# Optimization experiments

Hardware: AMD Instinct MI355X
Metric: run time of the kernel (lower is better)

## Reference

```python
import jax, jax.numpy as jnp
import numpy as np

N_NODES = 10000
N_EDGES = 160000
F_IN, D1, D2, D_OUT, K = 512, 512, 512, 256, 3


def _gcn_layer(x, row, col, w, W, b, n):
    # PyG GCNConv (improved=False): add self-loops with weight 1, sym norm.
    loop = jnp.arange(n)
    r = jnp.concatenate([row, loop])
    c = jnp.concatenate([col, loop])
    ww = jnp.concatenate([w, jnp.ones((n,), w.dtype)])
    deg = jax.ops.segment_sum(ww, c, num_segments=n)
    dinv = jnp.where(deg > 0, jax.lax.rsqrt(deg), 0.0)
    norm = dinv[r] * ww * dinv[c]              # [E+N]
    h = x @ W                                  # dense GEMM first (as PyG lin)
    out = jax.ops.segment_sum(norm[:, None] * h[r], c, num_segments=n)
    return out + b


def _cheb_layer(x, row, col, w, Wk, b, n):
    # PyG ChebConv, normalization='sym', lambda_max=2.0:
    # L_hat = 2L/lmax - I = -D^{-1/2} A D^{-1/2} (self-loops removed first).
    w0 = jnp.where(row == col, jnp.zeros((), w.dtype), w)  # remove self loops
    deg = jax.ops.segment_sum(w0, row, num_segments=n)
    dinv = jnp.where(deg > 0, jax.lax.rsqrt(deg), 0.0)
    norm = dinv[row] * w0 * dinv[col]          # [E]

    def lhat(z):  # L_hat @ z
        return -jax.ops.segment_sum(norm[:, None] * z[row], col, num_segments=n)

    Tx0 = x
    out = Tx0 @ Wk[0]
    Tx1 = lhat(x)
    out = out + Tx1 @ Wk[1]
    for k in range(2, Wk.shape[0]):            # static K, fine to unroll
        Tx2 = 2.0 * lhat(Tx1) - Tx0
        out = out + Tx2 @ Wk[k]
        Tx0, Tx1 = Tx1, Tx2
    return out + b


def setup_inputs() -> dict:
    key = jax.random.key(0)
    ks = jax.random.split(key, 9)
    x = jax.random.normal(ks[0], (N_NODES, F_IN), dtype=jnp.float32)
    edge_index = jax.random.randint(ks[1], (2, N_EDGES), 0, N_NODES, dtype=jnp.int64)
    edge_weight = jax.random.uniform(ks[2], (N_EDGES,), dtype=jnp.float32)
    s = lambda fan: 1.0 / np.sqrt(fan)
    W1 = jax.random.normal(ks[3], (F_IN, D1), dtype=jnp.float32) * s(F_IN)
    b1 = jnp.zeros((D1,), jnp.float32)
    W2 = jax.random.normal(ks[4], (D1, D2), dtype=jnp.float32) * s(D1)
    b2 = jnp.zeros((D2,), jnp.float32)
    Wc = jax.random.normal(ks[5], (K, D2, D_OUT), dtype=jnp.float32) * s(D2)
    bc = jnp.zeros((D_OUT,), jnp.float32)
    return {"x": x, "edge_index": edge_index, "edge_weight": edge_weight,
            "W1": W1, "b1": b1, "W2": W2, "b2": b2, "Wc": Wc, "bc": bc}


def reference(x, edge_index, edge_weight, W1, b1, W2, b2, Wc, bc):
    row, col = edge_index[0], edge_index[1]
    n = x.shape[0]
    h = jax.nn.celu(_gcn_layer(x, row, col, edge_weight, W1, b1, n))
    h = jax.nn.celu(_gcn_layer(h, row, col, edge_weight, W2, b2, n))
    h = jax.nn.celu(_cheb_layer(h, row, col, edge_weight, Wc, bc, n))
    return h
```

## Files before the change

kernel.cpp:

```cpp
#include <hip/hip_runtime.h>
#include <math.h>

#define N_NODES 10000
#define N_EDGES 160000
#define FDIM    512
#define DOUT    256
#define NCAT    768

typedef unsigned short ushort_t;
typedef unsigned int   uint_t;
typedef __attribute__((ext_vector_type(8))) short bf16x8;
typedef __attribute__((ext_vector_type(4))) float f32x4;

__device__ inline ushort_t f2bf(float f) {
    uint_t u = __float_as_uint(f);
    u += 0x7fffu + ((u >> 16) & 1u);
    return (ushort_t)(u >> 16);
}
__device__ inline void bf2f8(uint4 u, float* v) {
    v[0] = __uint_as_float(u.x << 16); v[1] = __uint_as_float(u.x & 0xffff0000u);
    v[2] = __uint_as_float(u.y << 16); v[3] = __uint_as_float(u.y & 0xffff0000u);
    v[4] = __uint_as_float(u.z << 16); v[5] = __uint_as_float(u.z & 0xffff0000u);
    v[6] = __uint_as_float(u.w << 16); v[7] = __uint_as_float(u.w & 0xffff0000u);
}
__device__ inline uint4 f2bf8v(const float* v) {
    uint4 u;
    u.x = (uint_t)f2bf(v[0]) | ((uint_t)f2bf(v[1]) << 16);
    u.y = (uint_t)f2bf(v[2]) | ((uint_t)f2bf(v[3]) << 16);
    u.z = (uint_t)f2bf(v[4]) | ((uint_t)f2bf(v[5]) << 16);
    u.w = (uint_t)f2bf(v[6]) | ((uint_t)f2bf(v[7]) << 16);
    return u;
}
__device__ inline void gld_lds16(const ushort_t* g, ushort_t* l) {
    __builtin_amdgcn_global_load_lds(
        (const __attribute__((address_space(1))) unsigned int*)g,
        (__attribute__((address_space(3))) unsigned int*)l,
        16, 0, 0);
}

#define EDGE_BLOCKS 625
#define XB_BLOCKS   5000

__global__ __launch_bounds__(256) void k_pre1(
    const int* __restrict__ row, const int* __restrict__ col,
    const float* __restrict__ w,
    float* deg_g, float* deg_c, int* counts,
    const float* __restrict__ x,  ushort_t* __restrict__ xb,
    const float* __restrict__ W1, ushort_t* __restrict__ W1t,
    const float* __restrict__ W2, ushort_t* __restrict__ W2t,
    const float* __restrict__ Wc, ushort_t* __restrict__ Wcatt)
{
    __shared__ float tile[64][65];
    int b = blockIdx.x;
    int tid = threadIdx.x;
    if (b < EDGE_BLOCKS) {
        int e = b * 256 + tid;
        if (e < N_EDGES) {
            int r = row[e], c = col[e];
            float wv = w[e];
            atomicAdd(&deg_g[c], wv);
            if (r != c) atomicAdd(&deg_c[r], wv);
            atomicAdd(&counts[c], 1);
        }
        return;
    }
    b -= EDGE_BLOCKS;
    if (b < XB_BLOCKS) {
        int t = b * 256 + tid;
        float4 v = *(const float4*)(x + (size_t)t * 4);
        uint2 p;
        p.x = (uint_t)f2bf(v.x) | ((uint_t)f2bf(v.y) << 16);
        p.y = (uint_t)f2bf(v.z) | ((uint_t)f2bf(v.w) << 16);
        *(uint2*)(xb + (size_t)t * 4) = p;
        return;
    }
    b -= XB_BLOCKS;
    const float* src; const float* src2 = nullptr;
    ushort_t* dst; int kt, ntG, srcld;
    if (b < 64) {
        kt = b >> 3; ntG = b & 7; srcld = FDIM;
        src = W1 + (size_t)(kt * 64) * FDIM + ntG * 64;
        dst = W1t;
    } else if (b < 128) {
        int bb = b - 64;
        kt = bb >> 3; ntG = bb & 7; srcld = FDIM;
        src = W2 + (size_t)(kt * 64) * FDIM + ntG * 64;
        dst = W2t;
    } else {
        int bb = b - 128;
        ntG = bb / 8; kt = bb % 8; srcld = DOUT;
        int s = ntG >> 2;
        int nl = (ntG & 3) * 64;
        if (s == 0) {
            src  = Wc + (size_t)(kt * 64) * DOUT + nl;
            src2 = Wc + (size_t)2 * FDIM * DOUT + (size_t)(kt * 64) * DOUT + nl;
        } else if (s == 1) {
            src  = Wc + (size_t)1 * FDIM * DOUT + (size_t)(kt * 64) * DOUT + nl;
        } else {
            src  = Wc + (size_t)2 * FDIM * DOUT + (size_t)(kt * 64) * DOUT + nl;
        }
        dst = Wcatt;
    }
    {
        int r = tid >> 2, c0 = (tid & 3) * 16;
        const float* sp = src + (size_t)r * srcld + c0;
#pragma unroll
        for (int q = 0; q < 4; ++q) {
            float4 a = *(const float4*)(sp + q * 4);
            if (src2) {
                float4 bsub = *(const float4*)(src2 + (size_t)r * srcld + c0 + q * 4);
                a.x -= bsub.x; a.y -= bsub.y; a.z -= bsub.z; a.w -= bsub.w;
            }
            tile[r][c0 + q * 4 + 0] = a.x;
            tile[r][c0 + q * 4 + 1] = a.y;
            tile[r][c0 + q * 4 + 2] = a.z;
            tile[r][c0 + q * 4 + 3] = a.w;
        }
    }
    __syncthreads();
    {
        int n = tid >> 2, k0 = (tid & 3) * 16;
        float v[16];
#pragma unroll
        for (int i = 0; i < 16; ++i) v[i] = tile[k0 + i][n];
        uint4 u0 = f2bf8v(v);
        uint4 u1 = f2bf8v(v + 8);
        ushort_t* dp = dst + (size_t)(ntG * 64 + n) * FDIM + kt * 64 + k0;
        *(uint4*)dp = u0;
        *(uint4*)(dp + 8) = u1;
    }
}

__global__ __launch_bounds__(256) void k_dinv_scan1(
    const float* __restrict__ deg_g, const float* __restrict__ deg_c,
    float* __restrict__ dinv_g, float* __restrict__ dinv_c,
    const int* __restrict__ counts, int* __restrict__ rp,
    int* __restrict__ part, int n)
{
    __shared__ int s[256];
    int tid = threadIdx.x;
    int i = blockIdx.x * 256 + tid;
    if (i < n) {
        dinv_g[i] = rsqrtf(deg_g[i] + 1.0f);
        float d = deg_c[i];
        dinv_c[i] = d > 0.f ? rsqrtf(d) : 0.f;
    }
    int v = (i < n) ? counts[i] : 0;
    s[tid] = v;
    __syncthreads();
    for (int o = 1; o < 256; o <<= 1) {
        int t = (tid >= o) ? s[tid - o] : 0;
        __syncthreads();
        s[tid] += t;
        __syncthreads();
    }
    if (i < n) rp[i] = s[tid] - v;
    if (tid == 255) part[blockIdx.x] = s[255];
}

__global__ __launch_bounds__(256) void k_scan23(int* __restrict__ rp,
                                                const int* __restrict__ part,
                                                int nb, int n) {
    __shared__ int soff[64];
    __shared__ int stot;
    int tid = threadIdx.x;
    if (tid < 64) {
        int v = (tid < nb) ? part[tid] : 0;
        int x = v;
        for (int o = 1; o < 64; o <<= 1) {
            int y = __shfl_up(x, o, 64);
            if (tid >= o) x += y;
        }
        soff[tid] = x - v;
        if (tid == 63) stot = x;
    }
    __syncthreads();
    int i = blockIdx.x * 256 + tid;
    if (i < n) rp[i] += soff[blockIdx.x];
    if (blockIdx.x == 0 && tid == 0) rp[n] = stot;
}

__global__ void k_fill(const int* __restrict__ row, const int* __restrict__ col,
                       const float* __restrict__ w,
                       const float* __restrict__ dinv_g, const float* __restrict__ dinv_c,
                       const int* __restrict__ rp, int* __restrict__ fill,
                       int2* __restrict__ eg, int2* __restrict__ ec, int E) {
    int e = blockIdx.x * blockDim.x + threadIdx.x;
    if (e >= E) return;
    int r = row[e], c = col[e];
    float wv = w[e];
    float ng = dinv_g[r] * wv * dinv_g[c];
    float w0 = (r == c) ? 0.f : wv;
    float nc = -(dinv_c[r] * w0 * dinv_c[c]);
    int pos = rp[c] + atomicAdd(&fill[c], 1);
    eg[pos] = make_int2(r, __float_as_int(ng));
    ec[pos] = make_int2(r, __float_as_int(nc));
}

__global__ __launch_bounds__(256) void k_mgemm(
    const ushort_t* __restrict__ A, int lda,
    const ushort_t* __restrict__ Bt, int ldb,
    int M, int K, int N, int nbx, int nby,
    ushort_t* __restrict__ outB)
{
    __shared__ ushort_t As[64 * 32];
    __shared__ ushort_t Bs[128 * 32];

    int id = blockIdx.x;
    int j = id & 7, t = id >> 3;
    int by = t % nby;
    int bx = (t / nby) * 8 + j;
    if (bx >= nbx) return;

    const int tid  = threadIdx.x;
    const int w    = tid >> 6;
    const int lane = tid & 63;
    const int l15  = lane & 15;
    const int quad = lane >> 4;
    const int bm = bx * 64, bn = by * 128;
    const int wm = (w & 1) * 32;
    const int wn = (w >> 1) * 64;

    const int sr = lane >> 2;
    const int sc = (lane & 3) * 8;
    int arow = min(bm + w * 16 + sr, M - 1);
    const ushort_t* ag = A + (size_t)arow * lda + sc;
    ushort_t* al = As + (w * 16 + sr) * 32 + sc;
    const ushort_t* bg0 = Bt + (size_t)(bn + w * 32 + sr) * ldb + sc;
    const ushort_t* bg1 = bg0 + (size_t)16 * ldb;
    ushort_t* bl0 = Bs + (w * 32 + sr) * 32 + sc;
    ushort_t* bl1 = bl0 + 16 * 32;

    f32x4 acc[2][4] = {};

    for (int k0 = 0; k0 < K; k0 += 32) {
        __syncthreads();
        gld_lds16(ag + k0, al);
        gld_lds16(bg0 + k0, bl0);
        gld_lds16(bg1 + k0, bl1);
        __syncthreads();
        bf16x8 af[2], bfr[4];
#pragma unroll
        for (int i = 0; i < 2; ++i)
            af[i] = *(const bf16x8*)(As + (wm + i * 16 + l15) * 32 + quad * 8);
#pragma unroll
        for (int jj = 0; jj < 4; ++jj)
            bfr[jj] = *(const bf16x8*)(Bs + (wn + jj * 16 + l15) * 32 + quad * 8);
#pragma unroll
        for (int i = 0; i < 2; ++i)
#pragma unroll
            for (int jj = 0; jj < 4; ++jj)
                acc[i][jj] = __builtin_amdgcn_mfma_f32_16x16x32_bf16(af[i], bfr[jj], acc[i][jj], 0, 0, 0);
    }

#pragma unroll
    for (int i = 0; i < 2; ++i) {
        int rowb = bm + wm + i * 16 + quad * 4;
#pragma unroll
        for (int jj = 0; jj < 4; ++jj) {
            int col = bn + wn + jj * 16 + l15;
#pragma unroll
            for (int r = 0; r < 4; ++r) {
                int rr = rowb + r;
                if (rr < M)
                    outB[(size_t)rr * N + col] = f2bf(acc[i][jj][r]);
            }
        }
    }
}

template<int SL>
__global__ __launch_bounds__(256) void k_sagg(
    const ushort_t* __restrict__ h, int hs, int hoff,
    const int2* __restrict__ er, const int* __restrict__ rp,
    const float* __restrict__ dinv_g,
    const ushort_t* __restrict__ other, int os, int ooff, float sB,
    const float* __restrict__ bias, float sA,
    ushort_t* __restrict__ outB, float* __restrict__ outF, int outs, int celu)
{
    const int id  = blockIdx.x;
    const int sl  = id % SL;
    const int tid = threadIdx.x;
    const int c   = (id / SL) * 32 + (tid >> 3);
    if (c >= N_NODES) return;
    const int f = sl * 64 + ((tid & 7) << 3);
    const ushort_t* hp = h + hoff + f;

    float acc[8] = {0.f, 0.f, 0.f, 0.f, 0.f, 0.f, 0.f, 0.f};
    int e = rp[c];
    const int e1 = rp[c + 1];
    for (; e + 4 <= e1; e += 4) {
        int2 p0 = er[e], p1 = er[e + 1], p2 = er[e + 2], p3 = er[e + 3];
        uint4 u0 = *(const uint4*)(hp + (size_t)p0.x * hs);
        uint4 u1 = *(const uint4*)(hp + (size_t)p1.x * hs);
        uint4 u2 = *(const uint4*)(hp + (size_t)p2.x * hs);
        uint4 u3 = *(const uint4*)(hp + (size_t)p3.x * hs);
        float n0 = __int_as_float(p0.y), n1 = __int_as_float(p1.y);
        float n2 = __int_as_float(p2.y), n3 = __int_as_float(p3.y);
        float v0[8], v1[8], v2[8], v3[8];
        bf2f8(u0, v0); bf2f8(u1, v1); bf2f8(u2, v2); bf2f8(u3, v3);
#pragma unroll
        for (int i = 0; i < 8; ++i) {
            acc[i] = fmaf(n0, v0[i], acc[i]);
            acc[i] = fmaf(n1, v1[i], acc[i]);
            acc[i] = fmaf(n2, v2[i], acc[i]);
            acc[i] = fmaf(n3, v3[i], acc[i]);
        }
    }
    for (; e < e1; ++e) {
        int2 p = er[e];
        uint4 u = *(const uint4*)(hp + (size_t)p.x * hs);
        float nv = __int_as_float(p.y);
        float v[8]; bf2f8(u, v);
#pragma unroll
        for (int i = 0; i < 8; ++i) acc[i] = fmaf(nv, v[i], acc[i]);
    }

    if (dinv_g) {
        float dv = dinv_g[c];
        float d2 = dv * dv;
        uint4 u = *(const uint4*)(hp + (size_t)c * hs);
        float v[8]; bf2f8(u, v);
#pragma unroll
        for (int i = 0; i < 8; ++i) acc[i] = fmaf(d2, v[i], acc[i]);
    }
    float r[8];
#pragma unroll
    for (int i = 0; i < 8; ++i) r[i] = sA * acc[i];
    if (other) {
        uint4 u = *(const uint4*)(other + (size_t)c * os + ooff + f);
        float o[8]; bf2f8(u, o);
#pragma unroll
        for (int i = 0; i < 8; ++i) r[i] = fmaf(sB, o[i], r[i]);
    }
    if (bias) {
#pragma unroll
        for (int i = 0; i < 8; ++i) r[i] += bias[f + i];
    }
    if (celu) {
#pragma unroll
        for (int i = 0; i < 8; ++i) r[i] = r[i] > 0.f ? r[i] : expm1f(r[i]);
    }
    if (outF) {
        float* op = outF + (size_t)c * outs + f;
        *(float4*)op       = make_float4(r[0], r[1], r[2], r[3]);
        *(float4*)(op + 4) = make_float4(r[4], r[5], r[6], r[7]);
    } else {
        *(uint4*)(outB + (size_t)c * outs + f) = f2bf8v(r);
    }
}


extern "C" void kernel_launch(void* const* d_in, const int* in_sizes, int n_in,
                              void* d_out, int out_size, void* d_ws, size_t ws_size,
                              hipStream_t stream) {
    const float* x  = (const float*)d_in[0];
    const int*   ei = (const int*)d_in[1];
    const float* ew = (const float*)d_in[2];
    const float* W1 = (const float*)d_in[3];
    const float* b1 = (const float*)d_in[4];
    const float* W2 = (const float*)d_in[5];
    const float* b2 = (const float*)d_in[6];
    const float* Wc = (const float*)d_in[7];
    const float* bc = (const float*)d_in[8];
    float* out = (float*)d_out;

    const int* row = ei;
    const int* col = ei + N_EDGES;

    char* ws = (char*)d_ws;
    size_t off = 0;
    auto alloc = [&](size_t bytes) -> void* {
        void* p = ws + off;
        off += (bytes + 255) & ~(size_t)255;
        return p;
    };
    ushort_t* xb    = (ushort_t*)alloc((size_t)N_NODES * FDIM * 2);
    ushort_t* bufA  = (ushort_t*)alloc((size_t)N_NODES * FDIM * 2);
    ushort_t* bufB  = (ushort_t*)alloc((size_t)N_NODES * FDIM * 2);
    ushort_t* Y     = (ushort_t*)alloc((size_t)N_NODES * NCAT * 2);
    ushort_t* P     = (ushort_t*)alloc((size_t)N_NODES * DOUT * 2);
    ushort_t* W1t   = (ushort_t*)alloc((size_t)FDIM * FDIM * 2);
    ushort_t* W2t   = (ushort_t*)alloc((size_t)FDIM * FDIM * 2);
    ushort_t* Wcatt = (ushort_t*)alloc((size_t)NCAT * FDIM * 2);
    size_t zs = off;
    float* deg_g  = (float*)alloc((size_t)N_NODES * 4);
    float* deg_c  = (float*)alloc((size_t)N_NODES * 4);
    int*   counts = (int*)alloc((size_t)N_NODES * 4);
    int*   fillb  = (int*)alloc((size_t)N_NODES * 4);
    size_t ze = off;
    float* dinv_g = (float*)alloc((size_t)N_NODES * 4);
    float* dinv_c = (float*)alloc((size_t)N_NODES * 4);
    int*   rp     = (int*)alloc((size_t)(N_NODES + 1) * 4);
    int*   part   = (int*)alloc(64 * 4);
    int2*  eg     = (int2*)alloc((size_t)N_EDGES * 8);
    int2*  ec     = (int2*)alloc((size_t)N_EDGES * 8);

    const int TB = 256;
    dim3 edgeGrid((N_EDGES + TB - 1) / TB);
    int nScanB = (N_NODES + 255) / 256;

    hipMemsetAsync(ws + zs, 0, ze - zs, stream);
    k_pre1<<<EDGE_BLOCKS + XB_BLOCKS + 224, 256, 0, stream>>>(
        row, col, ew, deg_g, deg_c, counts,
        x, xb, W1, W1t, W2, W2t, Wc, Wcatt);
    k_dinv_scan1<<<nScanB, 256, 0, stream>>>(deg_g, deg_c, dinv_g, dinv_c, counts, rp, part, N_NODES);
    k_scan23<<<nScanB, 256, 0, stream>>>(rp, part, nScanB, N_NODES);
    k_fill<<<edgeGrid, TB, 0, stream>>>(row, col, ew, dinv_g, dinv_c, rp, fillb, eg, ec, N_EDGES);

    auto mgemm = [&](const ushort_t* A, const ushort_t* Bt, int N, ushort_t* oB) {
        int nbx = (N_NODES + 63) / 64, nby = N / 128;
        int G = 8 * (((nbx + 7) / 8) * nby);
        k_mgemm<<<G, 256, 0, stream>>>(A, FDIM, Bt, FDIM, N_NODES, FDIM, N, nbx, nby, oB);
    };
    int g8 = ((N_NODES + 31) / 32) * 8;
    int g4 = ((N_NODES + 31) / 32) * 4;

    mgemm(xb, W1t, FDIM, bufA);
    k_sagg<8><<<g8, 256, 0, stream>>>(bufA, FDIM, 0, eg, rp, dinv_g,
                                      (const ushort_t*)nullptr, 0, 0, 0.f,
                                      b1, 1.f, bufB, (float*)nullptr, FDIM, 1);
    mgemm(bufB, W2t, FDIM, bufA);
    k_sagg<8><<<g8, 256, 0, stream>>>(bufA, FDIM, 0, eg, rp, dinv_g,
                                      (const ushort_t*)nullptr, 0, 0, 0.f,
                                      b2, 1.f, bufB, (float*)nullptr, FDIM, 1);
    mgemm(bufB, Wcatt, NCAT, Y);
    k_sagg<4><<<g4, 256, 0, stream>>>(Y, NCAT, 2 * DOUT, ec, rp,
                                      (const float*)nullptr,
                                      Y, NCAT, DOUT, 1.f,
                                      (const float*)nullptr, 2.f,
                                      P, (float*)nullptr, DOUT, 0);
    k_sagg<4><<<g4, 256, 0, stream>>>(P, DOUT, 0, ec, rp,
                                      (const float*)nullptr,
                                      Y, NCAT, 0, 1.f,
                                      bc, 1.f,
                                      (ushort_t*)nullptr, out, DOUT, 1);
}
```

Before: 239.7 us.

## Fuse all stages into one cooperative persistent megakernel with grid syncs

Replaces the sequence of preprocessing, GEMM and aggregation kernel launches with a single cooperative persistent kernel. Its blocks loop over virtual block ids and separate the phases with grid-wide barriers. A fallback multi-kernel path keeps grid-stride loops. The weight transpose tiles shrink from 64x64 to 32x32. The aim is to remove per-launch overhead and tail gaps between stages, at the cost of grid-sync latency, a grid capped at 1024 blocks that may lower GEMM occupancy or parallelism, and shared-memory and register limits set by the fused kernel.

Measured after the change: 905.3 us. +277.6%, slower.

```diff
diff --git a/kernel.cpp b/kernel.cpp
--- a/kernel.cpp
+++ b/kernel.cpp
@@ -1,11 +1,20 @@
 #include <hip/hip_runtime.h>
+#include <hip/hip_cooperative_groups.h>
 #include <math.h>
+
+namespace cg = cooperative_groups;
 
 #define N_NODES 10000
 #define N_EDGES 160000
 #define FDIM    512
 #define DOUT    256
 #define NCAT    768
+
+#define EDGE_BLOCKS 625
+#define XB_BLOCKS   5000
+#define TT_BLOCKS   896
+#define NSCANB      40
+#define SMEM_BYTES  12288
 
 typedef unsigned short ushort_t;
 typedef unsigned int   uint_t;
@@ -38,335 +47,399 @@
         16, 0, 0);
 }
 
-#define EDGE_BLOCKS 625
-#define XB_BLOCKS   5000
-
-__global__ __launch_bounds__(256) void k_pre1(
-    const int* __restrict__ row, const int* __restrict__ col,
-    const float* __restrict__ w,
-    float* deg_g, float* deg_c, int* counts,
-    const float* __restrict__ x,  ushort_t* __restrict__ xb,
-    const float* __restrict__ W1, ushort_t* __restrict__ W1t,
-    const float* __restrict__ W2, ushort_t* __restrict__ W2t,
-    const float* __restrict__ Wc, ushort_t* __restrict__ Wcatt)
+struct MegaArgs {
+    const int* row; const int* col; const float* ew;
+    const float* x;
+    const float* W1; const float* b1;
+    const float* W2; const float* b2;
+    const float* Wc; const float* bc;
+    float* out;
+    ushort_t* xb; ushort_t* bufA; ushort_t* bufB; ushort_t* Y; ushort_t* P;
+    ushort_t* W1t; ushort_t* W2t; ushort_t* Wcatt;
+    float* deg_g; float* deg_c; int* counts; int* fillb;
+    float* dinv_g; float* dinv_c; int* rp; int* part;
+    int2* eg; int2* ec;
+};
+
+__device__ __forceinline__ void phaseA(const MegaArgs& a, char* smem, int G) {
+    const int tid = threadIdx.x;
+    for (int vb = blockIdx.x; vb < EDGE_BLOCKS + XB_BLOCKS + TT_BLOCKS; vb += G) {
+        if (vb < EDGE_BLOCKS) {
+            int e = vb * 256 + tid;
+            int r = a.row[e], c = a.col[e];
+            float wv = a.ew[e];
+            atomicAdd(&a.deg_g[c], wv);
+            if (r != c) atomicAdd(&a.deg_c[r], wv);
+            atomicAdd(&a.counts[c], 1);
+        } else if (vb < EDGE_BLOCKS + XB_BLOCKS) {
+            int t = (vb - EDGE_BLOCKS) * 256 + tid;
+            float4 v = *(const float4*)(a.x + (size_t)t * 4);
+            uint2 p;
+            p.x = (uint_t)f2bf(v.x) | ((uint_t)f2bf(v.y) << 16);
+            p.y = (uint_t)f2bf(v.z) | ((uint_t)f2bf(v.w) << 16);
+            *(uint2*)(a.xb + (size_t)t * 4) = p;
+        } else {
+            int b = vb - EDGE_BLOCKS - XB_BLOCKS;
+            float (*tile)[33] = (float(*)[33])smem;
+            const float* src; const float* src2 = nullptr;
+            ushort_t* dst; int kt, nt, srcld, drb;
+            if (b < 256) {
+                kt = b >> 4; nt = b & 15; srcld = FDIM;
+                src = a.W1 + (size_t)(kt * 32) * FDIM + nt * 32;
+                dst = a.W1t; drb = nt * 32;
+            } else if (b < 512) {
+                int bb = b - 256;
+                kt = bb >> 4; nt = bb & 15; srcld = FDIM;
+                src = a.W2 + (size_t)(kt * 32) * FDIM + nt * 32;
+                dst = a.W2t; drb = nt * 32;
+            } else {
+                int bb = b - 512;
+                int sec = bb >> 7, tt = bb & 127;
+                kt = tt >> 3; nt = tt & 7; srcld = DOUT;
+                size_t o = (size_t)(kt * 32) * DOUT + nt * 32;
+                if (sec == 0) {
+                    src  = a.Wc + o;
+                    src2 = a.Wc + (size_t)2 * FDIM * DOUT + o;
+                } else if (sec == 1) {
+                    src  = a.Wc + (size_t)1 * FDIM * DOUT + o;
+                } else {
+                    src  = a.Wc + (size_t)2 * FDIM * DOUT + o;
+                }
+                dst = a.Wcatt; drb = sec * 256 + nt * 32;
+            }
+            {
+                int r = tid >> 3, c0 = (tid & 7) << 2;
+                float4 av = *(const float4*)(src + (size_t)r * srcld + c0);
+                if (src2) {
+                    float4 bs = *(const float4*)(src2 + (size_t)r * srcld + c0);
+                    av.x -= bs.x; av.y -= bs.y; av.z -= bs.z; av.w -= bs.w;
+                }
+                tile[r][c0 + 0] = av.x; tile[r][c0 + 1] = av.y;
+                tile[r][c0 + 2] = av.z; tile[r][c0 + 3] = av.w;
+            }
+            __syncthreads();
+            {
+                int n = tid >> 3, k0 = (tid & 7) << 2;
+                float v[4];
+#pragma unroll
+                for (int i = 0; i < 4; ++i) v[i] = tile[k0 + i][n];
+                uint2 p;
+                p.x = (uint_t)f2bf(v[0]) | ((uint_t)f2bf(v[1]) << 16);
+                p.y = (uint_t)f2bf(v[2]) | ((uint_t)f2bf(v[3]) << 16);
+                *(uint2*)(dst + (size_t)(drb + n) * FDIM + kt * 32 + k0) = p;
+            }
+            __syncthreads();
+        }
+    }
+}
+
+__device__ __forceinline__ void phaseB(const MegaArgs& a, char* smem, int G) {
+    const int tid = threadIdx.x;
+    int* s = (int*)smem;
+    for (int vb = blockIdx.x; vb < NSCANB; vb += G) {
+        int i = vb * 256 + tid;
+        if (i < N_NODES) {
+            a.dinv_g[i] = rsqrtf(a.deg_g[i] + 1.0f);
+            float d = a.deg_c[i];
+            a.dinv_c[i] = d > 0.f ? rsqrtf(d) : 0.f;
+        }
+        int v = (i < N_NODES) ? a.counts[i] : 0;
+        s[tid] = v;
+        __syncthreads();
+        for (int o = 1; o < 256; o <<= 1) {
+            int t2 = (tid >= o) ? s[tid - o] : 0;
+            __syncthreads();
+            s[tid] += t2;
+            __syncthreads();
+        }
+        if (i < N_NODES) a.rp[i] = s[tid] - v;
+        if (tid == 255) a.part[vb] = s[255];
+        __syncthreads();
+    }
+}
+
+__device__ __forceinline__ void phaseC(const MegaArgs& a, char* smem, int G) {
+    const int tid = threadIdx.x;
+    int* soff = (int*)smem;
+    for (int vb = blockIdx.x; vb < NSCANB; vb += G) {
+        if (tid < 64) {
+            int v = (tid < NSCANB) ? a.part[tid] : 0;
+            int x2 = v;
+            for (int o = 1; o < 64; o <<= 1) {
+                int y = __shfl_up(x2, o, 64);
+                if (tid >= o) x2 += y;
+            }
+            soff[tid] = x2 - v;
+            if (tid == 63) soff[63 + 1] = x2;
+        }
+        __syncthreads();
+        int i = vb * 256 + tid;
+        if (i < N_NODES) a.rp[i] += soff[vb];
+        if (vb == 0 && tid == 0) a.rp[N_NODES] = soff[64];
+        __syncthreads();
+    }
+}
+
+__device__ __forceinline__ void phaseD(const MegaArgs& a, int G) {
+    const int tid = threadIdx.x;
+    for (int vb = blockIdx.x; vb < EDGE_BLOCKS; vb += G) {
+        int e = vb * 256 + tid;
+        int r = a.row[e], c = a.col[e];
+        float wv = a.ew[e];
+        float ng = a.dinv_g[r] * wv * a.dinv_g[c];
+        float w0 = (r == c) ? 0.f : wv;
+        float nc = -(a.dinv_c[r] * w0 * a.dinv_c[c]);
+        int pos = a.rp[c] + atomicAdd(&a.fillb[c], 1);
+        a.eg[pos] = make_int2(r, __float_as_int(ng));
+        a.ec[pos] = make_int2(r, __float_as_int(nc));
+    }
+}
+
+__device__ __forceinline__ void gemmPhase(
+    const ushort_t* __restrict__ A, const ushort_t* __restrict__ Bt,
+    int N, ushort_t* __restrict__ outB, char* smem, int G)
 {
-    __shared__ float tile[64][65];
-    int b = blockIdx.x;
-    int tid = threadIdx.x;
-    if (b < EDGE_BLOCKS) {
-        int e = b * 256 + tid;
-        if (e < N_EDGES) {
-            int r = row[e], c = col[e];
-            float wv = w[e];
-            atomicAdd(&deg_g[c], wv);
-            if (r != c) atomicAdd(&deg_c[r], wv);
-            atomicAdd(&counts[c], 1);
-        }
-        return;
-    }
-    b -= EDGE_BLOCKS;
-    if (b < XB_BLOCKS) {
-        int t = b * 256 + tid;
-        float4 v = *(const float4*)(x + (size_t)t * 4);
-        uint2 p;
-        p.x = (uint_t)f2bf(v.x) | ((uint_t)f2bf(v.y) << 16);
-        p.y = (uint_t)f2bf(v.z) | ((uint_t)f2bf(v.w) << 16);
-        *(uint2*)(xb + (size_t)t * 4) = p;
-        return;
-    }
-    b -= XB_BLOCKS;
-    const float* src; const float* src2 = nullptr;
-    ushort_t* dst; int kt, ntG, srcld;
-    if (b < 64) {
-        kt = b >> 3; ntG = b & 7; srcld = FDIM;
-        src = W1 + (size_t)(kt * 64) * FDIM + ntG * 64;
-        dst = W1t;
-    } else if (b < 128) {
-        int bb = b - 64;
-        kt = bb >> 3; ntG = bb & 7; srcld = FDIM;
-        src = W2 + (size_t)(kt * 64) * FDIM + ntG * 64;
-        dst = W2t;
-    } else {
-        int bb = b - 128;
-        ntG = bb / 8; kt = bb % 8; srcld = DOUT;
-        int s = ntG >> 2;
-        int nl = (ntG & 3) * 64;
-        if (s == 0) {
-            src  = Wc + (size_t)(kt * 64) * DOUT + nl;
-            src2 = Wc + (size_t)2 * FDIM * DOUT + (size_t)(kt * 64) * DOUT + nl;
-        } else if (s == 1) {
-            src  = Wc + (size_t)1 * FDIM * DOUT + (size_t)(kt * 64) * DOUT + nl;
-        } else {
-            src  = Wc + (size_t)2 * FDIM * DOUT + (size_t)(kt * 64) * DOUT + nl;
-        }
-        dst = Wcatt;
-    }
-    {
-        int r = tid >> 2, c0 = (tid & 3) * 16;
-        const float* sp = src + (size_t)r * srcld + c0;
-#pragma unroll
-        for (int q = 0; q < 4; ++q) {
-            float4 a = *(const float4*)(sp + q * 4);
-            if (src2) {
-                float4 bsub = *(const float4*)(src2 + (size_t)r * srcld + c0 + q * 4);
-                a.x -= bsub.x; a.y -= bsub.y; a.z -= bsub.z; a.w -= bsub.w;
-            }
-            tile[r][c0 + q * 4 + 0] = a.x;
-            tile[r][c0 + q * 4 + 1] = a.y;
-            tile[r][c0 + q * 4 + 2] = a.z;
-            tile[r][c0 + q * 4 + 3] = a.w;
-        }
-    }
-    __syncthreads();
-    {
-        int n = tid >> 2, k0 = (tid & 3) * 16;
-        float v[16];
-#pragma unroll
-        for (int i = 0; i < 16; ++i) v[i] = tile[k0 + i][n];
-        uint4 u0 = f2bf8v(v);
-        uint4 u1 = f2bf8v(v + 8);
-        ushort_t* dp = dst + (size_t)(ntG * 64 + n) * FDIM + kt * 64 + k0;
-        *(uint4*)dp = u0;
-        *(uint4*)(dp + 8) = u1;
-    }
-}
-
-__global__ __launch_bounds__(256) void k_dinv_scan1(
-    const float* __restrict__ deg_g, const float* __restrict__ deg_c,
-    float* __restrict__ dinv_g, float* __restrict__ dinv_c,
-    const int* __restrict__ counts, int* __restrict__ rp,
-    int* __restrict__ part, int n)
-{
-    __shared__ int s[256];
-    int tid = threadIdx.x;
-    int i = blockIdx.x * 256 + tid;
-    if (i < n) {
-        dinv_g[i] = rsqrtf(deg_g[i] + 1.0f);
-        float d = deg_c[i];
-        dinv_c[i] = d > 0.f ? rsqrtf(d) : 0.f;
-    }
-    int v = (i < n) ? counts[i] : 0;
-    s[tid] = v;
-    __syncthreads();
-    for (int o = 1; o < 256; o <<= 1) {
-        int t = (tid >= o) ? s[tid - o] : 0;
-        __syncthreads();
-        s[tid] += t;
-        __syncthreads();
-    }
-    if (i < n) rp[i] = s[tid] - v;
-    if (tid == 255) part[blockIdx.x] = s[255];
-}
-
-__global__ __launch_bounds__(256) void k_scan23(int* __restrict__ rp,
-                                                const int* __restrict__ part,
-                                                int nb, int n) {
-    __shared__ int soff[64];
-    __shared__ int stot;
-    int tid = threadIdx.x;
-    if (tid < 64) {
-        int v = (tid < nb) ? part[tid] : 0;
-        int x = v;
-        for (int o = 1; o < 64; o <<= 1) {
-            int y = __shfl_up(x, o, 64);
-            if (tid >= o) x += y;
-        }
-        soff[tid] = x - v;
-        if (tid == 63) stot = x;
-    }
-    __syncthreads();
-    int i = blockIdx.x * 256 + tid;
-    if (i < n) rp[i] += soff[blockIdx.x];
-    if (blockIdx.x == 0 && tid == 0) rp[n] = stot;
-}
-
-__global__ void k_fill(const int* __restrict__ row, const int* __restrict__ col,
-                       const float* __restrict__ w,
-                       const float* __restrict__ dinv_g, const float* __restrict__ dinv_c,
-                       const int* __restrict__ rp, int* __restrict__ fill,
-                       int2* __restrict__ eg, int2* __restrict__ ec, int E) {
-    int e = blockIdx.x * blockDim.x + threadIdx.x;
-    if (e >= E) return;
-    int r = row[e], c = col[e];
-    float wv = w[e];
-    float ng = dinv_g[r] * wv * dinv_g[c];
-    float w0 = (r == c) ? 0.f : wv;
-    float nc = -(dinv_c[r] * w0 * dinv_c[c]);
-    int pos = rp[c] + atomicAdd(&fill[c], 1);
-    eg[pos] = make_int2(r, __float_as_int(ng));
-    ec[pos] = make_int2(r, __float_as_int(nc));
-}
-
-__global__ __launch_bounds__(256) void k_mgemm(
-    const ushort_t* __restrict__ A, int lda,
-    const ushort_t* __restrict__ Bt, int ldb,
-    int M, int K, int N, int nbx, int nby,
-    ushort_t* __restrict__ outB)
-{
-    __shared__ ushort_t As[64 * 32];
-    __shared__ ushort_t Bs[128 * 32];
-
-    int id = blockIdx.x;
-    int j = id & 7, t = id >> 3;
-    int by = t % nby;
-    int bx = (t / nby) * 8 + j;
-    if (bx >= nbx) return;
-
     const int tid  = threadIdx.x;
+    const int nby  = N >> 7;
+    const int nbx  = (N_NODES + 63) >> 6;
+    const int nvb  = 8 * (((nbx + 7) >> 3) * nby);
+    ushort_t* As = (ushort_t*)smem;
+    ushort_t* Bs = As + 64 * 32;
     const int w    = tid >> 6;
     const int lane = tid & 63;
     const int l15  = lane & 15;
     const int quad = lane >> 4;
-    const int bm = bx * 64, bn = by * 128;
-    const int wm = (w & 1) * 32;
-    const int wn = (w >> 1) * 64;
-
-    const int sr = lane >> 2;
-    const int sc = (lane & 3) * 8;
-    int arow = min(bm + w * 16 + sr, M - 1);
-    const ushort_t* ag = A + (size_t)arow * lda + sc;
-    ushort_t* al = As + (w * 16 + sr) * 32 + sc;
-    const ushort_t* bg0 = Bt + (size_t)(bn + w * 32 + sr) * ldb + sc;
-    const ushort_t* bg1 = bg0 + (size_t)16 * ldb;
-    ushort_t* bl0 = Bs + (w * 32 + sr) * 32 + sc;
-    ushort_t* bl1 = bl0 + 16 * 32;
-
-    f32x4 acc[2][4] = {};
-
-    for (int k0 = 0; k0 < K; k0 += 32) {
+    const int wm   = (w & 1) * 32;
+    const int wn   = (w >> 1) * 64;
+    const int sr   = lane >> 2;
+    const int sc   = (lane & 3) * 8;
+
+    for (int vb = blockIdx.x; vb < nvb; vb += G) {
+        int j = vb & 7, t = vb >> 3;
+        int by = t % nby;
+        int bx = (t / nby) * 8 + j;
+        if (bx >= nbx) continue;
+        const int bm = bx * 64, bn = by * 128;
+
+        int arow = min(bm + w * 16 + sr, N_NODES - 1);
+        const ushort_t* ag  = A + (size_t)arow * FDIM + sc;
+        ushort_t* al = As + (w * 16 + sr) * 32 + sc;
+        const ushort_t* bg0 = Bt + (size_t)(bn + w * 32 + sr) * FDIM + sc;
+        const ushort_t* bg1 = bg0 + (size_t)16 * FDIM;
+        ushort_t* bl0 = Bs + (w * 32 + sr) * 32 + sc;
+        ushort_t* bl1 = bl0 + 16 * 32;
+
+        f32x4 acc[2][4] = {};
+        for (int k0 = 0; k0 < FDIM; k0 += 32) {
+            __syncthreads();
+            gld_lds16(ag + k0, al);
+            gld_lds16(bg0 + k0, bl0);
+            gld_lds16(bg1 + k0, bl1);
+            __syncthreads();
+            bf16x8 af[2], bfr[4];
+#pragma unroll
+            for (int i = 0; i < 2; ++i)
+                af[i] = *(const bf16x8*)(As + (wm + i * 16 + l15) * 32 + quad * 8);
+#pragma unroll
+            for (int jj = 0; jj < 4; ++jj)
+                bfr[jj] = *(const bf16x8*)(Bs + (wn + jj * 16 + l15) * 32 + quad * 8);
+#pragma unroll
+            for (int i = 0; i < 2; ++i)
+#pragma unroll
+                for (int jj = 0; jj < 4; ++jj)
+                    acc[i][jj] = __builtin_amdgcn_mfma_f32_16x16x32_bf16(af[i], bfr[jj], acc[i][jj], 0, 0, 0);
+        }
         __syncthreads();
-        gld_lds16(ag + k0, al);
-        gld_lds16(bg0 + k0, bl0);
-        gld_lds16(bg1 + k0, bl1);
-        __syncthreads();
-        bf16x8 af[2], bfr[4];
-#pragma unroll
-        for (int i = 0; i < 2; ++i)
-            af[i] = *(const bf16x8*)(As + (wm + i * 16 + l15) * 32 + quad * 8);
-#pragma unroll
-        for (int jj = 0; jj < 4; ++jj)
-            bfr[jj] = *(const bf16x8*)(Bs + (wn + jj * 16 + l15) * 32 + quad * 8);
-#pragma unroll
-        for (int i = 0; i < 2; ++i)
-#pragma unroll
-            for (int jj = 0; jj < 4; ++jj)
-                acc[i][jj] = __builtin_amdgcn_mfma_f32_16x16x32_bf16(af[i], bfr[jj], acc[i][jj], 0, 0, 0);
-    }
-
-#pragma unroll
-    for (int i = 0; i < 2; ++i) {
-        int rowb = bm + wm + i * 16 + quad * 4;
-#pragma unroll
-        for (int jj = 0; jj < 4; ++jj) {
-            int col = bn + wn + jj * 16 + l15;
-#pragma unroll
-            for (int r = 0; r < 4; ++r) {
-                int rr = rowb + r;
-                if (rr < M)
-                    outB[(size_t)rr * N + col] = f2bf(acc[i][jj][r]);
+
+#pragma unroll
+        for (int i = 0; i < 2; ++i) {
+            int rowb = bm + wm + i * 16 + quad * 4;
+#pragma unroll
+            for (int jj = 0; jj < 4; ++jj) {
+                int col = bn + wn + jj * 16 + l15;
+#pragma unroll
+                for (int r = 0; r < 4; ++r) {
+                    int rr = rowb + r;
+                    if (rr < N_NODES)
+                        outB[(size_t)rr * N + col] = f2bf(acc[i][jj][r]);
+                }
             }
         }
     }
 }
 
 template<int SL>
-__global__ __launch_bounds__(256) void k_sagg(
+__device__ __forceinline__ void saggPhase(
     const ushort_t* __restrict__ h, int hs, int hoff,
     const int2* __restrict__ er, const int* __restrict__ rp,
     const float* __restrict__ dinv_g,
     const ushort_t* __restrict__ other, int os, int ooff, float sB,
     const float* __restrict__ bias, float sA,
-    ushort_t* __restrict__ outB, float* __restrict__ outF, int outs, int celu)
+    ushort_t* __restrict__ outB, float* __restrict__ outF, int outs, int celu,
+    int G)
 {
-    const int id  = blockIdx.x;
-    const int sl  = id % SL;
     const int tid = threadIdx.x;
-    const int c   = (id / SL) * 32 + (tid >> 3);
-    if (c >= N_NODES) return;
-    const int f = sl * 64 + ((tid & 7) << 3);
-    const ushort_t* hp = h + hoff + f;
-
-    float acc[8] = {0.f, 0.f, 0.f, 0.f, 0.f, 0.f, 0.f, 0.f};
-    int e = rp[c];
-    const int e1 = rp[c + 1];
-    for (; e + 4 <= e1; e += 4) {
-        int2 p0 = er[e], p1 = er[e + 1], p2 = er[e + 2], p3 = er[e + 3];
-        uint4 u0 = *(const uint4*)(hp + (size_t)p0.x * hs);
-        uint4 u1 = *(const uint4*)(hp + (size_t)p1.x * hs);
-        uint4 u2 = *(const uint4*)(hp + (size_t)p2.x * hs);
-        uint4 u3 = *(const uint4*)(hp + (size_t)p3.x * hs);
-        float n0 = __int_as_float(p0.y), n1 = __int_as_float(p1.y);
-        float n2 = __int_as_float(p2.y), n3 = __int_as_float(p3.y);
-        float v0[8], v1[8], v2[8], v3[8];
-        bf2f8(u0, v0); bf2f8(u1, v1); bf2f8(u2, v2); bf2f8(u3, v3);
-#pragma unroll
-        for (int i = 0; i < 8; ++i) {
-            acc[i] = fmaf(n0, v0[i], acc[i]);
-            acc[i] = fmaf(n1, v1[i], acc[i]);
-            acc[i] = fmaf(n2, v2[i], acc[i]);
-            acc[i] = fmaf(n3, v3[i], acc[i]);
-        }
-    }
-    for (; e < e1; ++e) {
-        int2 p = er[e];
-        uint4 u = *(const uint4*)(hp + (size_t)p.x * hs);
-        float nv = __int_as_float(p.y);
-        float v[8]; bf2f8(u, v);
-#pragma unroll
-        for (int i = 0; i < 8; ++i) acc[i] = fmaf(nv, v[i], acc[i]);
-    }
-
-    if (dinv_g) {
-        float dv = dinv_g[c];
-        float d2 = dv * dv;
-        uint4 u = *(const uint4*)(hp + (size_t)c * hs);
-        float v[8]; bf2f8(u, v);
-#pragma unroll
-        for (int i = 0; i < 8; ++i) acc[i] = fmaf(d2, v[i], acc[i]);
-    }
-    float r[8];
-#pragma unroll
-    for (int i = 0; i < 8; ++i) r[i] = sA * acc[i];
-    if (other) {
-        uint4 u = *(const uint4*)(other + (size_t)c * os + ooff + f);
-        float o[8]; bf2f8(u, o);
-#pragma unroll
-        for (int i = 0; i < 8; ++i) r[i] = fmaf(sB, o[i], r[i]);
-    }
-    if (bias) {
-#pragma unroll
-        for (int i = 0; i < 8; ++i) r[i] += bias[f + i];
-    }
-    if (celu) {
-#pragma unroll
-        for (int i = 0; i < 8; ++i) r[i] = r[i] > 0.f ? r[i] : expm1f(r[i]);
-    }
-    if (outF) {
-        float* op = outF + (size_t)c * outs + f;
-        *(float4*)op       = make_float4(r[0], r[1], r[2], r[3]);
-        *(float4*)(op + 4) = make_float4(r[4], r[5], r[6], r[7]);
-    } else {
-        *(uint4*)(outB + (size_t)c * outs + f) = f2bf8v(r);
-    }
+    const int nvb = ((N_NODES + 31) / 32) * SL;
+    for (int vb = blockIdx.x; vb < nvb; vb += G) {
+        const int sl = vb % SL;
+        const int c  = (vb / SL) * 32 + (tid >> 3);
+        if (c >= N_NODES) continue;
+        const int f = sl * 64 + ((tid & 7) << 3);
+        const ushort_t* hp = h + hoff + f;
+
+        float acc[8] = {0.f, 0.f, 0.f, 0.f, 0.f, 0.f, 0.f, 0.f};
+        int e = rp[c];
+        const int e1 = rp[c + 1];
+        for (; e + 4 <= e1; e += 4) {
+            int2 p0 = er[e], p1 = er[e + 1], p2 = er[e + 2], p3 = er[e + 3];
+            uint4 u0 = *(const uint4*)(hp + (size_t)p0.x * hs);
+            uint4 u1 = *(const uint4*)(hp + (size_t)p1.x * hs);
+            uint4 u2 = *(const uint4*)(hp + (size_t)p2.x * hs);
+            uint4 u3 = *(const uint4*)(hp + (size_t)p3.x * hs);
+            float n0 = __int_as_float(p0.y), n1 = __int_as_float(p1.y);
+            float n2 = __int_as_float(p2.y), n3 = __int_as_float(p3.y);
+            float v0[8], v1[8], v2[8], v3[8];
+            bf2f8(u0, v0); bf2f8(u1, v1); bf2f8(u2, v2); bf2f8(u3, v3);
+#pragma unroll
+            for (int i = 0; i < 8; ++i) {
+                acc[i] = fmaf(n0, v0[i], acc[i]);
+                acc[i] = fmaf(n1, v1[i], acc[i]);
+                acc[i] = fmaf(n2, v2[i], acc[i]);
+                acc[i] = fmaf(n3, v3[i], acc[i]);
+            }
+        }
+        for (; e < e1; ++e) {
+            int2 p = er[e];
+            uint4 u = *(const uint4*)(hp + (size_t)p.x * hs);
+            float nv = __int_as_float(p.y);
+            float v[8]; bf2f8(u, v);
+#pragma unroll
+            for (int i = 0; i < 8; ++i) acc[i] = fmaf(nv, v[i], acc[i]);
+        }
+
+        if (dinv_g) {
+            float dv = dinv_g[c];
+            float d2 = dv * dv;
+            uint4 u = *(const uint4*)(hp + (size_t)c * hs);
+            float v[8]; bf2f8(u, v);
+#pragma unroll
+            for (int i = 0; i < 8; ++i) acc[i] = fmaf(d2, v[i], acc[i]);
+        }
+        float r[8];
+#pragma unroll
+        for (int i = 0; i < 8; ++i) r[i] = sA * acc[i];
+        if (other) {
+            uint4 u = *(const uint4*)(other + (size_t)c * os + ooff + f);
+            float o[8]; bf2f8(u, o);
+#pragma unroll
+            for (int i = 0; i < 8; ++i) r[i] = fmaf(sB, o[i], r[i]);
+        }
+        if (bias) {
+#pragma unroll
+            for (int i = 0; i < 8; ++i) r[i] += bias[f + i];
+        }
+        if (celu) {
+#pragma unroll
+            for (int i = 0; i < 8; ++i) r[i] = r[i] > 0.f ? r[i] : expm1f(r[i]);
+        }
+        if (outF) {
+            float* op = outF + (size_t)c * outs + f;
+            *(float4*)op       = make_float4(r[0], r[1], r[2], r[3]);
+            *(float4*)(op + 4) = make_float4(r[4], r[5], r[6], r[7]);
+        } else {
+            *(uint4*)(outB + (size_t)c * outs + f) = f2bf8v(r);
+        }
+    }
+}
+
+__global__ __launch_bounds__(256, 4) void k_mega(MegaArgs a)
+{
+    __shared__ __align__(16) char smem[SMEM_BYTES];
+    const int G = gridDim.x;
+    cg::grid_group grid = cg::this_grid();
+
+    phaseA(a, smem, G);
+    grid.sync();
+    phaseB(a, smem, G);
+    grid.sync();
+    phaseC(a, smem, G);
+    grid.sync();
+    phaseD(a, G);
+    grid.sync();
+
+    gemmPhase(a.xb, a.W1t, FDIM, a.bufA, smem, G);
+    grid.sync();
+    saggPhase<8>(a.bufA, FDIM, 0, a.eg, a.rp, a.dinv_g,
+                 (const ushort_t*)nullptr, 0, 0, 0.f,
+                 a.b1, 1.f, a.bufB, (float*)nullptr, FDIM, 1, G);
+    grid.sync();
+    gemmPhase(a.bufB, a.W2t, FDIM, a.bufA, smem, G);
+    grid.sync();
+    saggPhase<8>(a.bufA, FDIM, 0, a.eg, a.rp, a.dinv_g,
+                 (const ushort_t*)nullptr, 0, 0, 0.f,
+                 a.b2, 1.f, a.bufB, (float*)nullptr, FDIM, 1, G);
+    grid.sync();
+    gemmPhase(a.bufB, a.Wcatt, NCAT, a.Y, smem, G);
+    grid.sync();
+    saggPhase<4>(a.Y, NCAT, 2 * DOUT, a.ec, a.rp,
+                 (const float*)nullptr,
+                 a.Y, NCAT, DOUT, 1.f,
+                 (const float*)nullptr, 2.f,
+                 a.P, (float*)nullptr, DOUT, 0, G);
+    grid.sync();
+    saggPhase<4>(a.P, DOUT, 0, a.ec, a.rp,
+                 (const float*)nullptr,
+                 a.Y, NCAT, 0, 1.f,
+                 a.bc, 1.f,
+                 (ushort_t*)nullptr, a.out, DOUT, 1, G);
+}
+
+__global__ __launch_bounds__(256) void k_phaseA(MegaArgs a) {
+    __shared__ __align__(16) char smem[SMEM_BYTES];
+    phaseA(a, smem, gridDim.x);
+}
+__global__ __launch_bounds__(256) void k_phaseB(MegaArgs a) {
+    __shared__ __align__(16) char smem[SMEM_BYTES];
+    phaseB(a, smem, gridDim.x);
+}
+__global__ __launch_bounds__(256) void k_phaseC(MegaArgs a) {
+    __shared__ __align__(16) char smem[SMEM_BYTES];
+    phaseC(a, smem, gridDim.x);
+}
+__global__ __launch_bounds__(256) void k_phaseD(MegaArgs a) {
+    phaseD(a, gridDim.x);
+}
+__global__ __launch_bounds__(256) void k_gemmW(
+    const ushort_t* A, const ushort_t* Bt, int N, ushort_t* outB) {
+    __shared__ __align__(16) char smem[SMEM_BYTES];
+    gemmPhase(A, Bt, N, outB, smem, gridDim.x);
+}
+template<int SL>
+__global__ __launch_bounds__(256) void k_saggW(
+    const ushort_t* h, int hs, int hoff, const int2* er, const int* rp,
+    const float* dinv_g, const ushort_t* other, int os, int ooff, float sB,
+    const float* bias, float sA, ushort_t* outB, float* outF, int outs, int celu) {
+    saggPhase<SL>(h, hs, hoff, er, rp, dinv_g, other, os, ooff, sB,
+                  bias, sA, outB, outF, outs, celu, gridDim.x);
 }
 
 
 extern "C" void kernel_launch(void* const* d_in, const int* in_sizes, int n_in,
                               void* d_out, int out_size, void* d_ws, size_t ws_size,
                               hipStream_t stream) {
-    const float* x  = (const float*)d_in[0];
-    const int*   ei = (const int*)d_in[1];
-    const float* ew = (const float*)d_in[2];
-    const float* W1 = (const float*)d_in[3];
-    const float* b1 = (const float*)d_in[4];
-    const float* W2 = (const float*)d_in[5];
-    const float* b2 = (const float*)d_in[6];
-    const float* Wc = (const float*)d_in[7];
-    const float* bc = (const float*)d_in[8];
-    float* out = (float*)d_out;
-
-    const int* row = ei;
-    const int* col = ei + N_EDGES;
+    MegaArgs a;
+    a.x  = (const float*)d_in[0];
+    const int* ei = (const int*)d_in[1];
+    a.ew = (const float*)d_in[2];
+    a.W1 = (const float*)d_in[3];
+    a.b1 = (const float*)d_in[4];
+    a.W2 = (const float*)d_in[5];
+    a.b2 = (const float*)d_in[6];
+    a.Wc = (const float*)d_in[7];
+    a.bc = (const float*)d_in[8];
+    a.out = (float*)d_out;
+    a.row = ei;
+    a.col = ei + N_EDGES;
 
     char* ws = (char*)d_ws;
     size_t off = 0;
@@ -375,64 +448,65 @@
         off += (bytes + 255) & ~(size_t)255;
         return p;
     };
-    ushort_t* xb    = (ushort_t*)alloc((size_t)N_NODES * FDIM * 2);
-    ushort_t* bufA  = (ushort_t*)alloc((size_t)N_NODES * FDIM * 2);
-    ushort_t* bufB  = (ushort_t*)alloc((size_t)N_NODES * FDIM * 2);
-    ushort_t* Y     = (ushort_t*)alloc((size_t)N_NODES * NCAT * 2);
-    ushort_t* P     = (ushort_t*)alloc((size_t)N_NODES * DOUT * 2);
-    ushort_t* W1t   = (ushort_t*)alloc((size_t)FDIM * FDIM * 2);
-    ushort_t* W2t   = (ushort_t*)alloc((size_t)FDIM * FDIM * 2);
-    ushort_t* Wcatt = (ushort_t*)alloc((size_t)NCAT * FDIM * 2);
+    a.xb    = (ushort_t*)alloc((size_t)N_NODES * FDIM * 2);
+    a.bufA  = (ushort_t*)alloc((size_t)N_NODES * FDIM * 2);
+    a.bufB  = (ushort_t*)alloc((size_t)N_NODES * FDIM * 2);
+    a.Y     = (ushort_t*)alloc((size_t)N_NODES * NCAT * 2);
+    a.P     = (ushort_t*)alloc((size_t)N_NODES * DOUT * 2);
+    a.W1t   = (ushort_t*)alloc((size_t)FDIM * FDIM * 2);
+    a.W2t   = (ushort_t*)alloc((size_t)FDIM * FDIM * 2);
+    a.Wcatt = (ushort_t*)alloc((size_t)NCAT * FDIM * 2);
     size_t zs = off;
-    float* deg_g  = (float*)alloc((size_t)N_NODES * 4);
-    float* deg_c  = (float*)alloc((size_t)N_NODES * 4);
-    int*   counts = (int*)alloc((size_t)N_NODES * 4);
-    int*   fillb  = (int*)alloc((size_t)N_NODES * 4);
+    a.deg_g  = (float*)alloc((size_t)N_NODES * 4);
+    a.deg_c  = (float*)alloc((size_t)N_NODES * 4);
+    a.counts = (int*)alloc((size_t)N_NODES * 4);
+    a.fillb  = (int*)alloc((size_t)N_NODES * 4);
     size_t ze = off;
-    float* dinv_g = (float*)alloc((size_t)N_NODES * 4);
-    float* dinv_c = (float*)alloc((size_t)N_NODES * 4);
-    int*   rp     = (int*)alloc((size_t)(N_NODES + 1) * 4);
-    int*   part   = (int*)alloc(64 * 4);
-    int2*  eg     = (int2*)alloc((size_t)N_EDGES * 8);
-    int2*  ec     = (int2*)alloc((size_t)N_EDGES * 8);
-
-    const int TB = 256;
-    dim3 edgeGrid((N_EDGES + TB - 1) / TB);
-    int nScanB = (N_NODES + 255) / 256;
+    a.dinv_g = (float*)alloc((size_t)N_NODES * 4);
+    a.dinv_c = (float*)alloc((size_t)N_NODES * 4);
+    a.rp     = (int*)alloc((size_t)(N_NODES + 1) * 4);
+    a.part   = (int*)alloc(64 * 4);
+    a.eg     = (int2*)alloc((size_t)N_EDGES * 8);
+    a.ec     = (int2*)alloc((size_t)N_EDGES * 8);
 
     hipMemsetAsync(ws + zs, 0, ze - zs, stream);
-    k_pre1<<<EDGE_BLOCKS + XB_BLOCKS + 224, 256, 0, stream>>>(
-        row, col, ew, deg_g, deg_c, counts,
-        x, xb, W1, W1t, W2, W2t, Wc, Wcatt);
-    k_dinv_scan1<<<nScanB, 256, 0, stream>>>(deg_g, deg_c, dinv_g, dinv_c, counts, rp, part, N_NODES);
-    k_scan23<<<nScanB, 256, 0, stream>>>(rp, part, nScanB, N_NODES);
-    k_fill<<<edgeGrid, TB, 0, stream>>>(row, col, ew, dinv_g, dinv_c, rp, fillb, eg, ec, N_EDGES);
-
-    auto mgemm = [&](const ushort_t* A, const ushort_t* Bt, int N, ushort_t* oB) {
-        int nbx = (N_NODES + 63) / 64, nby = N / 128;
-        int G = 8 * (((nbx + 7) / 8) * nby);
-        k_mgemm<<<G, 256, 0, stream>>>(A, FDIM, Bt, FDIM, N_NODES, FDIM, N, nbx, nby, oB);
-    };
-    int g8 = ((N_NODES + 31) / 32) * 8;
-    int g4 = ((N_NODES + 31) / 32) * 4;
-
-    mgemm(xb, W1t, FDIM, bufA);
-    k_sagg<8><<<g8, 256, 0, stream>>>(bufA, FDIM, 0, eg, rp, dinv_g,
-                                      (const ushort_t*)nullptr, 0, 0, 0.f,
-                                      b1, 1.f, bufB, (float*)nullptr, FDIM, 1);
-    mgemm(bufB, W2t, FDIM, bufA);
-    k_sagg<8><<<g8, 256, 0, stream>>>(bufA, FDIM, 0, eg, rp, dinv_g,
-                                      (const ushort_t*)nullptr, 0, 0, 0.f,
-                                      b2, 1.f, bufB, (float*)nullptr, FDIM, 1);
-    mgemm(bufB, Wcatt, NCAT, Y);
-    k_sagg<4><<<g4, 256, 0, stream>>>(Y, NCAT, 2 * DOUT, ec, rp,
-                                      (const float*)nullptr,
-                                      Y, NCAT, DOUT, 1.f,
-                                      (const float*)nullptr, 2.f,
-                                      P, (float*)nullptr, DOUT, 0);
-    k_sagg<4><<<g4, 256, 0, stream>>>(P, DOUT, 0, ec, rp,
-                                      (const float*)nullptr,
-                                      Y, NCAT, 0, 1.f,
-                                      bc, 1.f,
-                                      (ushort_t*)nullptr, out, DOUT, 1);
-}
+
+    int maxB = 0;
+    hipError_t qerr = hipOccupancyMaxActiveBlocksPerMultiprocessor(&maxB, k_mega, 256, 0);
+    int G = 0;
+    if (qerr == hipSuccess && maxB > 0) {
+        G = maxB * 256;
+        if (G > 1024) G = 1024;
+        G &= ~7;
+    }
+
+    if (G >= 256) {
+        void* params[] = { &a };
+        hipLaunchCooperativeKernel((void*)k_mega, dim3(G), dim3(256),
+                                   params, 0, stream);
+    } else {
+        k_phaseA<<<EDGE_BLOCKS + XB_BLOCKS + TT_BLOCKS, 256, 0, stream>>>(a);
+        k_phaseB<<<NSCANB, 256, 0, stream>>>(a);
+        k_phaseC<<<NSCANB, 256, 0, stream>>>(a);
+        k_phaseD<<<EDGE_BLOCKS, 256, 0, stream>>>(a);
+        k_gemmW<<<640, 256, 0, stream>>>(a.xb, a.W1t, FDIM, a.bufA);
+        k_saggW<8><<<2504, 256, 0, stream>>>(a.bufA, FDIM, 0, a.eg, a.rp, a.dinv_g,
+                                             (const ushort_t*)nullptr, 0, 0, 0.f,
+                                             a.b1, 1.f, a.bufB, (float*)nullptr, FDIM, 1);
+        k_gemmW<<<640, 256, 0, stream>>>(a.bufB, a.W2t, FDIM, a.bufA);
+        k_saggW<8><<<2504, 256, 0, stream>>>(a.bufA, FDIM, 0, a.eg, a.rp, a.dinv_g,
+                                             (const ushort_t*)nullptr, 0, 0, 0.f,
+                                             a.b2, 1.f, a.bufB, (float*)nullptr, FDIM, 1);
+        k_gemmW<<<960, 256, 0, stream>>>(a.bufB, a.Wcatt, NCAT, a.Y);
+        k_saggW<4><<<1252, 256, 0, stream>>>(a.Y, NCAT, 2 * DOUT, a.ec, a.rp,
+                                             (const float*)nullptr,
+                                             a.Y, NCAT, DOUT, 1.f,
+                                             (const float*)nullptr, 2.f,
+                                             a.P, (float*)nullptr, DOUT, 0);
+        k_saggW<4><<<1252, 256, 0, stream>>>(a.P, DOUT, 0, a.ec, a.rp,
+                                             (const float*)nullptr,
+                                             a.Y, NCAT, 0, 1.f,
+                                             a.bc, 1.f,
+                                             (ushort_t*)nullptr, a.out, DOUT, 1);
+    }
+}
```
